# Kernel optimization log

Measured on AMD Instinct MI355X. Metric: run time of the kernel, lower is better.

## Reference

```python
import jax, jax.numpy as jnp
import numpy as np

N = 100000
N1 = 12500  # N // K clusters after one downsample
K = 8
CHANNELS = [256, 128, 64, 32, 3]


def _conv(f, idx, kern, bias, act):
    # gather K neighbors and flatten: [M, K*Cin]
    g = f[idx].reshape(idx.shape[0], -1)
    out = g @ kern.T + bias
    return jax.nn.sigmoid(out) if act else out


def setup_inputs() -> dict:
    key = jax.random.key(0)
    ks = jax.random.split(key, 16)
    inp = {
        "features": jax.random.normal(ks[0], (N, 256), dtype=jnp.float32),
        "knn_idx0": jax.random.randint(ks[1], (N, K), 0, N, dtype=jnp.int32),
        "knn_idx1": jax.random.randint(ks[2], (N1, K), 0, N1, dtype=jnp.int32),
        "labels": jax.random.randint(ks[3], (N,), 0, N1, dtype=jnp.int32),
    }
    cin = 256
    for i, cout in enumerate(CHANNELS):
        inp[f"k{i}"] = jax.random.normal(ks[4 + i], (cout, K * cin), dtype=jnp.float32) * 0.1
        inp[f"b{i}"] = jnp.zeros((1, cout), dtype=jnp.float32)
        cin = cout
    return inp


def reference(features, knn_idx0, knn_idx1, labels, k0, b0, k1, b1, k2, b2, k3, b3, k4, b4):
    f = features
    # layer 0 (full resolution)
    f = _conv(f, knn_idx0, k0, b0, act=True)
    # layer 1: downsample via scatter-mean over kmeans labels
    s = jax.ops.segment_sum(f, labels, num_segments=N1)
    cnt = jax.ops.segment_sum(jnp.ones((f.shape[0], 1), f.dtype), labels, num_segments=N1)
    f = s / jnp.maximum(cnt, 1.0)
    f = _conv(f, knn_idx1, k1, b1, act=True)
    # layer 2 (coarse resolution)
    f = _conv(f, knn_idx1, k2, b2, act=True)
    # layer 3: upsample by indexing cluster features back to points
    f = f[labels]
    f = _conv(f, knn_idx0, k3, b3, act=True)
    # layer 4: final, no sigmoid
    f = _conv(f, knn_idx0, k4, b4, act=False)
    return f
```

## Files before the change

kernel.cpp:

```cpp
#include <hip/hip_runtime.h>
#include <hip/hip_bf16.h>


typedef __attribute__((ext_vector_type(8))) _Float16 f16x8;
typedef __attribute__((ext_vector_type(4))) float f32x4;
typedef __attribute__((ext_vector_type(8))) unsigned short u16x8;

#define NPTS 100000
#define N1PTS 12500

__device__ __forceinline__ void gload_lds16(const unsigned short* g, unsigned short* l) {
  __builtin_amdgcn_global_load_lds(
      (const __attribute__((address_space(1))) void*)g,
      (__attribute__((address_space(3))) void*)l, 16, 0, 0);
}

__device__ __forceinline__ int swz(int r, int k) {
  return r * 64 + ((((k >> 3) ^ r) & 7) << 3) + (k & 7);
}

__device__ __forceinline__ unsigned short f16bits(float x) {
  return __builtin_bit_cast(unsigned short, (_Float16)x);
}

__global__ void prepack_w(const float* __restrict__ W, unsigned short* __restrict__ out,
                          int n) {
  int i = blockIdx.x * 256 + threadIdx.x;
  if (i < n) out[i] = f16bits(W[i]);
}

__global__ void prepack_w0(const float* __restrict__ W, unsigned short* __restrict__ out) {
  const int tid = blockIdx.x * 256 + threadIdx.x;
  const int l = tid & 63;
  const int s = (tid >> 6) & 1;
  const int n = (tid >> 7) & 3;
  const int w = (tid >> 9) & 3;
  const int c = tid >> 11;
  const int co = w * 64 + n * 16 + (l & 15);
  const int k = c * 64 + s * 32 + ((l >> 4) << 3);
  const float* src = W + (size_t)co * 2048 + k;
  u16x8 h;
#pragma unroll
  for (int e = 0; e < 8; ++e) h[e] = f16bits(src[e]);
  ((u16x8*)out)[tid] = h;
}

__global__ void prepack_feat(const float* __restrict__ F, unsigned short* __restrict__ out,
                             int n8) {
  int i = blockIdx.x * 256 + threadIdx.x;
  if (i >= n8) return;
  const float4* s = (const float4*)(F + (size_t)i * 8);
  float4 v0 = s[0], v1 = s[1];
  float x[8] = {v0.x, v0.y, v0.z, v0.w, v1.x, v1.y, v1.z, v1.w};
  u16x8 o;
#pragma unroll
  for (int e = 0; e < 8; ++e) o[e] = f16bits(x[e]);
  ((u16x8*)out)[i] = o;
}

__global__ void count_labels(const int* __restrict__ labels, int* __restrict__ cnt) {
  int i = blockIdx.x * 256 + threadIdx.x;
  if (i < NPTS) atomicAdd(&cnt[labels[i]], 1);
}

__global__ void compose_idx(const int* __restrict__ knn0, const int* __restrict__ labels,
                            int* __restrict__ out) {
  int i = blockIdx.x * 256 + threadIdx.x;
  if (i < NPTS * 8) out[i] = labels[knn0[i]];
}

__global__ void finalize_pool(const int* __restrict__ pool, const int* __restrict__ cnt,
                              unsigned short* __restrict__ out) {
  int i = blockIdx.x * 256 + threadIdx.x;
  if (i >= N1PTS * 256) return;
  float denom = fmaxf((float)cnt[i >> 8], 1.0f);
  out[i] = f16bits(((float)pool[i]) * (1.0f / 16777216.0f) / denom);
}

__global__ __launch_bounds__(256, 3) void conv0_gemm(
    const unsigned short* __restrict__ F16, const int* __restrict__ idx,
    const int* __restrict__ lab, const unsigned short* __restrict__ Wpk,
    const float* __restrict__ bias, int* __restrict__ pool) {
  __shared__ alignas(16) unsigned short sA[4][64 * 64];

  const int t = threadIdx.x;
  const int w = t >> 6, l = t & 63;
  const int lr = l & 15, lh = l >> 4;
  const int row0 = blockIdx.x * 64;

  const int srow8 = l >> 3;
  const int sseg_src = (l & 7) ^ (srow8 & 7);

  const unsigned ldsbase = (unsigned)(uintptr_t)&sA[0][0];
  unsigned aoff[4][2];
#pragma unroll
  for (int m = 0; m < 4; ++m)
#pragma unroll
    for (int s = 0; s < 2; ++s)
      aoff[m][s] =
          ldsbase + (((m * 16 + lr) * 64 + ((((s << 2) + lh) ^ (lr & 7)) << 3)) << 1);

  auto ldnb = [&](int cc, int q) -> int {
    int grow = row0 + w * 16 + q * 8 + srow8;
    grow = grow < NPTS ? grow : NPTS - 1;
    return idx[grow * 8 + ((cc & 31) >> 2)];
  };
  auto stage_q = [&](int cc, int nb, int q) {
    const unsigned short* gp =
        F16 + ((size_t)nb << 8) + ((cc & 3) << 6) + sseg_src * 8;
    unsigned short* lp = &sA[cc & 3][(w * 16 + q * 8) * 64];
    gload_lds16(gp, lp);
  };
  auto loadB = [&](int cc, f16x8 (&bh)[2][4]) {
#pragma unroll
    for (int s = 0; s < 2; ++s)
#pragma unroll
      for (int n = 0; n < 4; ++n)
        bh[s][n] = *(const f16x8*)(
            Wpk + ((((size_t)cc * 4 + w) * 4 + n) * 2 + s) * 512 + (size_t)l * 8);
  };

  f32x4 acc[4][4] = {};
  f16x8 bh[2][4];

  int n00 = ldnb(0, 0), n01 = ldnb(0, 1);
  int n10 = ldnb(1, 0), n11 = ldnb(1, 1);
  int nc0 = ldnb(2, 0), nc1 = ldnb(2, 1);
  loadB(0, bh);
  stage_q(0, n00, 0); stage_q(0, n01, 1);
  stage_q(1, n10, 0); stage_q(1, n11, 1);
  __builtin_amdgcn_sched_barrier(0);
  asm volatile("s_waitcnt vmcnt(2)" ::: "memory");
  __builtin_amdgcn_sched_barrier(0);
  __builtin_amdgcn_s_barrier();
  __builtin_amdgcn_sched_barrier(0);

#pragma unroll 1
  for (int c = 0; c < 32; ++c) {
    const unsigned bb = (unsigned)((c & 3) << 13);

    f16x8 av[4][2];
    asm volatile("ds_read_b128 %0, %1" : "=v"(av[0][0]) : "v"(aoff[0][0] + bb));
    asm volatile("ds_read_b128 %0, %1" : "=v"(av[1][0]) : "v"(aoff[1][0] + bb));
    asm volatile("ds_read_b128 %0, %1" : "=v"(av[2][0]) : "v"(aoff[2][0] + bb));
    asm volatile("ds_read_b128 %0, %1" : "=v"(av[3][0]) : "v"(aoff[3][0] + bb));
    asm volatile("ds_read_b128 %0, %1" : "=v"(av[0][1]) : "v"(aoff[0][1] + bb));
    asm volatile("ds_read_b128 %0, %1" : "=v"(av[1][1]) : "v"(aoff[1][1] + bb));
    asm volatile("ds_read_b128 %0, %1" : "=v"(av[2][1]) : "v"(aoff[2][1] + bb));
    asm volatile("ds_read_b128 %0, %1" : "=v"(av[3][1]) : "v"(aoff[3][1] + bb));
    asm volatile("s_waitcnt lgkmcnt(0)");
    __builtin_amdgcn_sched_barrier(0);

    f16x8 bnext[2][4];
    loadB((c + 1) & 31, bnext);
#pragma unroll
    for (int s = 0; s < 2; ++s)
#pragma unroll
      for (int n = 0; n < 4; ++n)
#pragma unroll
        for (int m = 0; m < 4; ++m)
          acc[m][n] =
              __builtin_amdgcn_mfma_f32_16x16x32_f16(av[m][s], bh[s][n], acc[m][n], 0, 0, 0);
#pragma unroll
    for (int s = 0; s < 2; ++s)
#pragma unroll
      for (int n = 0; n < 4; ++n)
        bh[s][n] = bnext[s][n];
    __builtin_amdgcn_sched_barrier(0);

    const int cn = (c + 3) & 31;
    int t0 = ldnb(cn, 0), t1 = ldnb(cn, 1);
    const int cg = (c + 2) & 31;
    stage_q(cg, nc0, 0); stage_q(cg, nc1, 1);
    __builtin_amdgcn_sched_barrier(0);
    asm volatile("s_waitcnt vmcnt(12)" ::: "memory");
    __builtin_amdgcn_sched_barrier(0);
    __builtin_amdgcn_s_barrier();
    __builtin_amdgcn_sched_barrier(0);
    nc0 = t0; nc1 = t1;
  }
  asm volatile("s_waitcnt vmcnt(0)" ::: "memory");

  float bv[4];
#pragma unroll
  for (int n = 0; n < 4; ++n) bv[n] = bias[w * 64 + n * 16 + lr];
#pragma unroll
  for (int m = 0; m < 4; ++m) {
#pragma unroll
    for (int r = 0; r < 4; ++r) {
      const int i = row0 + m * 16 + lh * 4 + r;
      if (i < NPTS) {
        const int lb = lab[i];
#pragma unroll
        for (int n = 0; n < 4; ++n) {
          float z = acc[m][n][r] + bv[n];
          z = 1.0f / (1.0f + expf(-z));
          atomicAdd(&pool[(size_t)lb * 256 + (w * 64 + n * 16 + lr)],
                    __float2int_rn(z * 16777216.0f));
        }
      }
    }
  }
}

template <bool ACT, bool OUT16>
__global__ __launch_bounds__(256, 2) void conv_gemm(
    const unsigned short* __restrict__ act16, const int* __restrict__ idx,
    const unsigned short* __restrict__ Wf, const float* __restrict__ bias,
    void* __restrict__ outp, int M, int cinShift, int Cout, int Ktot) {
  __shared__ alignas(16) unsigned short sAh[4096];
  __shared__ alignas(16) unsigned short sBh[4096];

  const int Cin = 1 << cinShift;
  const int t = threadIdx.x;
  const int bm = blockIdx.x, bn = blockIdx.y;

  const int sr = t >> 2;
  const int kseg = (t & 3) << 4;
  const int ai = bm * 64 + sr;
  const int bco = bn * 64 + sr;

  f32x4 acc[4] = {};

  const int nch = Ktot >> 6;
  for (int kc = 0; kc < nch; ++kc) {
    const int kg = (kc << 6) + kseg;

    u16x8 h0 = {}, h1 = {};
    if (ai < M) {
      const int j = kg >> cinShift;
      const int nbv = idx[ai * 8 + j];
      const unsigned short* src = act16 + ((size_t)nbv << cinShift) + (kg & (Cin - 1));
      h0 = ((const u16x8*)src)[0];
      h1 = ((const u16x8*)src)[1];
    }

    u16x8 bh0 = {}, bh1 = {};
    if (bco < Cout) {
      const unsigned short* sw = Wf + (size_t)bco * Ktot + kg;
      bh0 = ((const u16x8*)sw)[0];
      bh1 = ((const u16x8*)sw)[1];
    }

    __syncthreads();
    const int w0 = swz(sr, kseg), w1 = swz(sr, kseg + 8);
    *(u16x8*)&sAh[w0] = h0; *(u16x8*)&sAh[w1] = h1;
    *(u16x8*)&sBh[w0] = bh0; *(u16x8*)&sBh[w1] = bh1;
    __syncthreads();

    const int l = t & 63;
    const int lr = l & 15, lh = l >> 4;
    const int wid = t >> 6;
#pragma unroll
    for (int s = 0; s < 2; ++s) {
      const int kb = s * 32 + lh * 8;
      const int boff = swz(wid * 16 + lr, kb);
      f16x8 bh = *(const f16x8*)&sBh[boff];
#pragma unroll
      for (int m = 0; m < 4; ++m) {
        const int aoff = swz(m * 16 + lr, kb);
        f16x8 ah = *(const f16x8*)&sAh[aoff];
        acc[m] = __builtin_amdgcn_mfma_f32_16x16x32_f16(ah, bh, acc[m], 0, 0, 0);
      }
    }
  }

  const int l = t & 63, wid = t >> 6;
  const int lr = l & 15, lh = l >> 4;
  const int co = bn * 64 + wid * 16 + lr;
  if (co < Cout) {
    const float bvv = bias[co];
#pragma unroll
    for (int m = 0; m < 4; ++m) {
#pragma unroll
      for (int r = 0; r < 4; ++r) {
        const int i = bm * 64 + m * 16 + lh * 4 + r;
        if (i < M) {
          float z = acc[m][r] + bvv;
          if (ACT) z = 1.0f / (1.0f + expf(-z));
          if (OUT16)
            ((unsigned short*)outp)[(size_t)i * Cout + co] = f16bits(z);
          else
            ((float*)outp)[(size_t)i * Cout + co] = z;
        }
      }
    }
  }
}

extern "C" void kernel_launch(void* const* d_in, const int* in_sizes, int n_in,
                              void* d_out, int out_size, void* d_ws, size_t ws_size,
                              hipStream_t stream) {
  const float* features = (const float*)d_in[0];
  const int* knn0 = (const int*)d_in[1];
  const int* knn1 = (const int*)d_in[2];
  const int* labels = (const int*)d_in[3];
  const float* kw[5] = {(const float*)d_in[4], (const float*)d_in[6],
                        (const float*)d_in[8], (const float*)d_in[10],
                        (const float*)d_in[12]};
  const float* bw[5] = {(const float*)d_in[5], (const float*)d_in[7],
                        (const float*)d_in[9], (const float*)d_in[11],
                        (const float*)d_in[13]};

  char* ws = (char*)d_ws;
  size_t off = 0;
  auto alloc = [&](size_t bytes) -> void* {
    void* p = ws + off;
    off = (off + bytes + 255) & ~(size_t)255;
    return p;
  };
  unsigned short* Wpk0 = (unsigned short*)alloc((size_t)524288 * 2);
  const int wsz14[4] = {262144, 65536, 16384, 768};
  const int woff14[4] = {0, 262144, 327680, 344064};
  unsigned short* W14 = (unsigned short*)alloc((size_t)344832 * 2);
  int* pool = (int*)alloc((size_t)N1PTS * 256 * 4);
  int* cnt = (int*)alloc((size_t)N1PTS * 4);
  unsigned short* pooled = (unsigned short*)alloc((size_t)N1PTS * 256 * 2);
  unsigned short* f1 = (unsigned short*)alloc((size_t)N1PTS * 128 * 2);
  unsigned short* f2 = (unsigned short*)alloc((size_t)N1PTS * 64 * 2);
  int* idx3 = (int*)alloc((size_t)NPTS * 8 * 4);
  unsigned short* F16 = (unsigned short*)alloc((size_t)NPTS * 256 * 2);
  unsigned short* f3 = (unsigned short*)pool;
  if (off > ws_size) return;

  prepack_w0<<<256, 256, 0, stream>>>(kw[0], Wpk0);
  for (int i = 0; i < 4; ++i)
    prepack_w<<<(wsz14[i] + 255) / 256, 256, 0, stream>>>(kw[i + 1], W14 + woff14[i], wsz14[i]);
  prepack_feat<<<(NPTS * 256 / 8 + 255) / 256, 256, 0, stream>>>(features, F16, NPTS * 256 / 8);
  compose_idx<<<(NPTS * 8 + 255) / 256, 256, 0, stream>>>(knn0, labels, idx3);

  hipMemsetAsync(pool, 0, (size_t)N1PTS * 256 * 4 + (size_t)N1PTS * 4, stream);
  count_labels<<<(NPTS + 255) / 256, 256, 0, stream>>>(labels, cnt);

  conv0_gemm<<<1563, 256, 0, stream>>>(F16, knn0, labels, Wpk0, bw[0], pool);

  finalize_pool<<<(N1PTS * 256 + 255) / 256, 256, 0, stream>>>(pool, cnt, pooled);

  dim3 blk(256);
  conv_gemm<true, true><<<dim3(196, 2), blk, 0, stream>>>(
      pooled, knn1, W14 + woff14[0], bw[1], f1, N1PTS, 8, 128, 2048);
  conv_gemm<true, true><<<dim3(196, 1), blk, 0, stream>>>(
      f1, knn1, W14 + woff14[1], bw[2], f2, N1PTS, 7, 64, 1024);
  conv_gemm<true, true><<<dim3(1563, 1), blk, 0, stream>>>(
      f2, idx3, W14 + woff14[2], bw[3], f3, NPTS, 6, 32, 512);
  conv_gemm<false, false><<<dim3(1563, 1), blk, 0, stream>>>(
      f3, knn0, W14 + woff14[3], bw[4], (float*)d_out, NPTS, 5, 3, 256);
}
```

Before: 302.3 us.

## Split-K the coarse conv layers with atomic int accumulation and retune conv0 pipelining

The two coarse-resolution convolutions (12500 rows) now run a 4-way split-K. Each slice atomically adds fixed-point integer partial sums into a zeroed buffer, and a separate finalize kernel applies bias and sigmoid. The goal is to fill the GPU, since the old grid had only 196 to 392 blocks. The conv0 main loop is also restructured so the first half of the MFMAs starts after a partial LDS wait (lgkmcnt(4)), with weight loads issued through a simple pointer-stride walk. The costs are two extra launches, atomic traffic, a larger memset, and fixed-point quantization of the layer outputs.

```diff
diff --git a/kernel.cpp b/kernel.cpp
--- a/kernel.cpp
+++ b/kernel.cpp
@@ -77,6 +77,14 @@
   out[i] = f16bits(((float)pool[i]) * (1.0f / 16777216.0f) / denom);
 }
 
+__global__ void finalize_splitk(const int* __restrict__ acc, const float* __restrict__ bias,
+                                unsigned short* __restrict__ out, int n, int cmask) {
+  int i = blockIdx.x * 256 + threadIdx.x;
+  if (i >= n) return;
+  float z = ((float)acc[i]) * (1.0f / 4194304.0f) + bias[i & cmask];
+  out[i] = f16bits(1.0f / (1.0f + expf(-z)));
+}
+
 __global__ __launch_bounds__(256, 3) void conv0_gemm(
     const unsigned short* __restrict__ F16, const int* __restrict__ idx,
     const int* __restrict__ lab, const unsigned short* __restrict__ Wpk,
@@ -99,6 +107,8 @@
     for (int s = 0; s < 2; ++s)
       aoff[m][s] =
           ldsbase + (((m * 16 + lr) * 64 + ((((s << 2) + lh) ^ (lr & 7)) << 3)) << 1);
+
+  const f16x8* wp8 = (const f16x8*)Wpk + (size_t)w * 512 + l;
 
   auto ldnb = [&](int cc, int q) -> int {
     int grow = row0 + w * 16 + q * 8 + srow8;
@@ -111,14 +121,6 @@
     unsigned short* lp = &sA[cc & 3][(w * 16 + q * 8) * 64];
     gload_lds16(gp, lp);
   };
-  auto loadB = [&](int cc, f16x8 (&bh)[2][4]) {
-#pragma unroll
-    for (int s = 0; s < 2; ++s)
-#pragma unroll
-      for (int n = 0; n < 4; ++n)
-        bh[s][n] = *(const f16x8*)(
-            Wpk + ((((size_t)cc * 4 + w) * 4 + n) * 2 + s) * 512 + (size_t)l * 8);
-  };
 
   f32x4 acc[4][4] = {};
   f16x8 bh[2][4];
@@ -126,8 +128,14 @@
   int n00 = ldnb(0, 0), n01 = ldnb(0, 1);
   int n10 = ldnb(1, 0), n11 = ldnb(1, 1);
   int nc0 = ldnb(2, 0), nc1 = ldnb(2, 1);
-  loadB(0, bh);
+  __builtin_amdgcn_sched_barrier(0);
+#pragma unroll
+  for (int s = 0; s < 2; ++s)
+#pragma unroll
+    for (int n = 0; n < 4; ++n) bh[s][n] = wp8[n * 128 + s * 64];
+  __builtin_amdgcn_sched_barrier(0);
   stage_q(0, n00, 0); stage_q(0, n01, 1);
+  __builtin_amdgcn_sched_barrier(0);
   stage_q(1, n10, 0); stage_q(1, n11, 1);
   __builtin_amdgcn_sched_barrier(0);
   asm volatile("s_waitcnt vmcnt(2)" ::: "memory");
@@ -148,28 +156,40 @@
     asm volatile("ds_read_b128 %0, %1" : "=v"(av[1][1]) : "v"(aoff[1][1] + bb));
     asm volatile("ds_read_b128 %0, %1" : "=v"(av[2][1]) : "v"(aoff[2][1] + bb));
     asm volatile("ds_read_b128 %0, %1" : "=v"(av[3][1]) : "v"(aoff[3][1] + bb));
+    __builtin_amdgcn_sched_barrier(0);
+    asm volatile("s_waitcnt lgkmcnt(4)");
+    __builtin_amdgcn_sched_barrier(0);
+
+    const f16x8* wpn = wp8 + 2048;
+    f16x8 bnext[2][4];
+#pragma unroll
+    for (int s = 0; s < 2; ++s)
+#pragma unroll
+      for (int n = 0; n < 4; ++n) bnext[s][n] = wpn[n * 128 + s * 64];
+#pragma unroll
+    for (int n = 0; n < 4; ++n)
+#pragma unroll
+      for (int m = 0; m < 4; ++m)
+        acc[m][n] =
+            __builtin_amdgcn_mfma_f32_16x16x32_f16(av[m][0], bh[0][n], acc[m][n], 0, 0, 0);
+    __builtin_amdgcn_sched_barrier(0);
     asm volatile("s_waitcnt lgkmcnt(0)");
     __builtin_amdgcn_sched_barrier(0);
-
-    f16x8 bnext[2][4];
-    loadB((c + 1) & 31, bnext);
+#pragma unroll
+    for (int n = 0; n < 4; ++n)
+#pragma unroll
+      for (int m = 0; m < 4; ++m)
+        acc[m][n] =
+            __builtin_amdgcn_mfma_f32_16x16x32_f16(av[m][1], bh[1][n], acc[m][n], 0, 0, 0);
 #pragma unroll
     for (int s = 0; s < 2; ++s)
 #pragma unroll
-      for (int n = 0; n < 4; ++n)
-#pragma unroll
-        for (int m = 0; m < 4; ++m)
-          acc[m][n] =
-              __builtin_amdgcn_mfma_f32_16x16x32_f16(av[m][s], bh[s][n], acc[m][n], 0, 0, 0);
-#pragma unroll
-    for (int s = 0; s < 2; ++s)
-#pragma unroll
-      for (int n = 0; n < 4; ++n)
-        bh[s][n] = bnext[s][n];
+      for (int n = 0; n < 4; ++n) bh[s][n] = bnext[s][n];
     __builtin_amdgcn_sched_barrier(0);
 
     const int cn = (c + 3) & 31;
     int t0 = ldnb(cn, 0), t1 = ldnb(cn, 1);
+    __builtin_amdgcn_sched_barrier(0);
     const int cg = (c + 2) & 31;
     stage_q(cg, nc0, 0); stage_q(cg, nc1, 1);
     __builtin_amdgcn_sched_barrier(0);
@@ -178,6 +198,7 @@
     __builtin_amdgcn_s_barrier();
     __builtin_amdgcn_sched_barrier(0);
     nc0 = t0; nc1 = t1;
+    wp8 = wpn;
   }
   asm volatile("s_waitcnt vmcnt(0)" ::: "memory");
 
@@ -203,17 +224,18 @@
   }
 }
 
-template <bool ACT, bool OUT16>
+template <bool ACT, bool OUT16, bool SPLITK>
 __global__ __launch_bounds__(256, 2) void conv_gemm(
     const unsigned short* __restrict__ act16, const int* __restrict__ idx,
     const unsigned short* __restrict__ Wf, const float* __restrict__ bias,
-    void* __restrict__ outp, int M, int cinShift, int Cout, int Ktot) {
+    void* __restrict__ outp, int M, int cinShift, int Cout, int Ktot, int ksl) {
   __shared__ alignas(16) unsigned short sAh[4096];
   __shared__ alignas(16) unsigned short sBh[4096];
 
   const int Cin = 1 << cinShift;
   const int t = threadIdx.x;
   const int bm = blockIdx.x, bn = blockIdx.y;
+  const int kbase = SPLITK ? blockIdx.z * ksl : 0;
 
   const int sr = t >> 2;
   const int kseg = (t & 3) << 4;
@@ -222,9 +244,9 @@
 
   f32x4 acc[4] = {};
 
-  const int nch = Ktot >> 6;
+  const int nch = ksl >> 6;
   for (int kc = 0; kc < nch; ++kc) {
-    const int kg = (kc << 6) + kseg;
+    const int kg = kbase + (kc << 6) + kseg;
 
     u16x8 h0 = {}, h1 = {};
     if (ai < M) {
@@ -269,7 +291,7 @@
   const int lr = l & 15, lh = l >> 4;
   const int co = bn * 64 + wid * 16 + lr;
   if (co < Cout) {
-    const float bvv = bias[co];
+    const float bvv = SPLITK ? 0.0f : bias[co];
 #pragma unroll
     for (int m = 0; m < 4; ++m) {
 #pragma unroll
@@ -277,11 +299,16 @@
         const int i = bm * 64 + m * 16 + lh * 4 + r;
         if (i < M) {
           float z = acc[m][r] + bvv;
-          if (ACT) z = 1.0f / (1.0f + expf(-z));
-          if (OUT16)
-            ((unsigned short*)outp)[(size_t)i * Cout + co] = f16bits(z);
-          else
-            ((float*)outp)[(size_t)i * Cout + co] = z;
+          if (SPLITK) {
+            atomicAdd(&((int*)outp)[(size_t)i * Cout + co],
+                      __float2int_rn(z * 4194304.0f));
+          } else {
+            if (ACT) z = 1.0f / (1.0f + expf(-z));
+            if (OUT16)
+              ((unsigned short*)outp)[(size_t)i * Cout + co] = f16bits(z);
+            else
+              ((float*)outp)[(size_t)i * Cout + co] = z;
+          }
         }
       }
     }
@@ -309,12 +336,14 @@
     off = (off + bytes + 255) & ~(size_t)255;
     return p;
   };
-  unsigned short* Wpk0 = (unsigned short*)alloc((size_t)524288 * 2);
+  unsigned short* Wpk0 = (unsigned short*)alloc((size_t)(524288 + 16384) * 2);
   const int wsz14[4] = {262144, 65536, 16384, 768};
   const int woff14[4] = {0, 262144, 327680, 344064};
   unsigned short* W14 = (unsigned short*)alloc((size_t)344832 * 2);
   int* pool = (int*)alloc((size_t)N1PTS * 256 * 4);
   int* cnt = (int*)alloc((size_t)N1PTS * 4);
+  int* f1i = (int*)alloc((size_t)N1PTS * 128 * 4);
+  int* f2i = (int*)alloc((size_t)N1PTS * 64 * 4);
   unsigned short* pooled = (unsigned short*)alloc((size_t)N1PTS * 256 * 2);
   unsigned short* f1 = (unsigned short*)alloc((size_t)N1PTS * 128 * 2);
   unsigned short* f2 = (unsigned short*)alloc((size_t)N1PTS * 64 * 2);
@@ -329,7 +358,7 @@
   prepack_feat<<<(NPTS * 256 / 8 + 255) / 256, 256, 0, stream>>>(features, F16, NPTS * 256 / 8);
   compose_idx<<<(NPTS * 8 + 255) / 256, 256, 0, stream>>>(knn0, labels, idx3);
 
-  hipMemsetAsync(pool, 0, (size_t)N1PTS * 256 * 4 + (size_t)N1PTS * 4, stream);
+  hipMemsetAsync(pool, 0, (size_t)((char*)pooled - (char*)pool), stream);
   count_labels<<<(NPTS + 255) / 256, 256, 0, stream>>>(labels, cnt);
 
   conv0_gemm<<<1563, 256, 0, stream>>>(F16, knn0, labels, Wpk0, bw[0], pool);
@@ -337,12 +366,16 @@
   finalize_pool<<<(N1PTS * 256 + 255) / 256, 256, 0, stream>>>(pool, cnt, pooled);
 
   dim3 blk(256);
-  conv_gemm<true, true><<<dim3(196, 2), blk, 0, stream>>>(
-      pooled, knn1, W14 + woff14[0], bw[1], f1, N1PTS, 8, 128, 2048);
-  conv_gemm<true, true><<<dim3(196, 1), blk, 0, stream>>>(
-      f1, knn1, W14 + woff14[1], bw[2], f2, N1PTS, 7, 64, 1024);
-  conv_gemm<true, true><<<dim3(1563, 1), blk, 0, stream>>>(
-      f2, idx3, W14 + woff14[2], bw[3], f3, NPTS, 6, 32, 512);
-  conv_gemm<false, false><<<dim3(1563, 1), blk, 0, stream>>>(
-      f3, knn0, W14 + woff14[3], bw[4], (float*)d_out, NPTS, 5, 3, 256);
-}
+  conv_gemm<true, true, true><<<dim3(196, 2, 4), blk, 0, stream>>>(
+      pooled, knn1, W14 + woff14[0], bw[1], f1i, N1PTS, 8, 128, 2048, 512);
+  finalize_splitk<<<(N1PTS * 128 + 255) / 256, 256, 0, stream>>>(
+      f1i, bw[1], f1, N1PTS * 128, 127);
+  conv_gemm<true, true, true><<<dim3(196, 1, 4), blk, 0, stream>>>(
+      f1, knn1, W14 + woff14[1], bw[2], f2i, N1PTS, 7, 64, 1024, 256);
+  finalize_splitk<<<(N1PTS * 64 + 255) / 256, 256, 0, stream>>>(
+      f2i, bw[2], f2, N1PTS * 64, 63);
+  conv_gemm<true, true, false><<<dim3(1563, 1), blk, 0, stream>>>(
+      f2, idx3, W14 + woff14[2], bw[3], f3, NPTS, 6, 32, 512, 512);
+  conv_gemm<false, false, false><<<dim3(1563, 1), blk, 0, stream>>>(
+      f3, knn0, W14 + woff14[3], bw[4], (float*)d_out, NPTS, 5, 3, 256, 256);
+}
```

Result: no change. 298.7 us (-1.2%).
